# Performance work log

Measured on AMD Instinct MI355X. Metric: run time of the kernel, lower is better.

Reference implementation:

```python
import jax, jax.numpy as jnp
import numpy as np
from jax.scipy.linalg import solve_triangular

B, L, HID, H = 2, 2048, 1024, 4
DK, DV = HID // H, HID // H
CHUNK = 32
CONV_K, FIR_SK, FIR_LK, FIR_WK = 4, 3, 31, 64
GIN = HID + 15 * H   # gate mlp input dim
GH = 2 * HID         # fusion_hidden_mult * hidden
FLOOR_INIT = float(np.log(0.05 / 0.95))


def _l2norm(x):
    return x / jnp.sqrt(jnp.sum(x * x, -1, keepdims=True) + 1e-6)


def _dwconv_causal(x_blc, w_ck):
    # x: [B,L,C], w: [C,K] depthwise causal FIR along L
    K = w_ck.shape[-1]
    x = jnp.moveaxis(x_blc, 1, 2)                      # [B,C,L]
    x = jnp.pad(x, ((0, 0), (0, 0), (K - 1, 0)))
    y = jax.lax.conv_general_dilated(x, w_ck[:, None, :], (1,), 'VALID',
                                     feature_group_count=w_ck.shape[0],
                                     dimension_numbers=('NCH', 'OIH', 'NCH'))
    return jnp.moveaxis(y, 2, 1)


def _delta_rule(q, k, v, beta):
    # q,k: [b,h,L,dk]; v: [b,h,L,dv]; beta: [b,h,L]; L % CHUNK == 0
    b, h, Ll, dk = q.shape
    dv = v.shape[-1]
    n = Ll // CHUNK
    q = _l2norm(q); k = _l2norm(k)
    v = v * beta[..., None]
    kb = k * beta[..., None]
    rs = lambda t: t.reshape(b, h, n, CHUNK, t.shape[-1])
    q, k, v, kb = rs(q), rs(k), rs(v), rs(kb)
    tril_strict = jnp.tril(jnp.ones((CHUNK, CHUNK), bool), -1)
    tril = jnp.tril(jnp.ones((CHUNK, CHUNK), bool), 0)
    # strictly-lower part of (k_beta k^T); inv = (I + A)^{-1} (unit lower-triangular)
    A = jnp.where(tril_strict, kb @ jnp.swapaxes(k, -1, -2), 0.0)
    eye = jnp.eye(CHUNK, dtype=q.dtype)
    inv = solve_triangular(eye + A, jnp.broadcast_to(eye, A.shape), lower=True)
    u = inv @ v    # [b,h,n,c,dv]
    w = inv @ kb   # [b,h,n,c,dk]
    qs, ks, us, ws = (jnp.moveaxis(t, 2, 0) for t in (q, k, u, w))
    S0 = jnp.zeros((b, h, dk, dv), q.dtype)

    def step(S, xs):
        q_i, k_i, u_i, w_i = xs
        attn = jnp.where(tril, q_i @ jnp.swapaxes(k_i, -1, -2), 0.0)
        u_adj = u_i - w_i @ S
        o_i = q_i @ S + attn @ u_adj
        S = S + jnp.swapaxes(k_i, -1, -2) @ u_adj
        return S, o_i

    S, o = jax.lax.scan(step, S0, (qs, ks, us, ws))
    o = jnp.moveaxis(o, 0, 2).reshape(b, h, Ll, dv)
    return o, S


def _stats(x):
    # x: [b,l,h,d] -> concat(mean, rms, max_abs) over d -> [b,l,3h]
    mean = x.mean(-1)
    rms = jnp.sqrt(jnp.clip(jnp.mean(x * x, -1), 1e-8))
    mx = jnp.abs(x).max(-1)
    return jnp.concatenate([mean, rms, mx], -1)


def _forward(hidden_states, q_w, k_w, v_w, b_w, convq_w, convk_w, convv_w,
             fir_s, fir_l, fir_wd, g1_w, g1_b, g2_w, g2_b,
             value_bias, log_temp, floor_logit, onorm_w, o_w):
    b, Ll, _ = hidden_states.shape
    # projections + causal short conv + silu (qk_activation='silu')
    q = jax.nn.silu(_dwconv_causal(hidden_states @ q_w.T, convq_w))
    k = jax.nn.silu(_dwconv_causal(hidden_states @ k_w.T, convk_w))
    v = jax.nn.silu(_dwconv_causal(hidden_states @ v_w.T, convv_w))
    tohd = lambda t: t.reshape(b, Ll, H, -1)
    q, k, v = tohd(q), tohd(k), tohd(v)
    beta = jax.nn.sigmoid(hidden_states @ b_w.T)            # [b,l,h]
    tr = lambda t: jnp.moveaxis(t, 1, 2)
    delta_out, _S = _delta_rule(tr(q), tr(k), tr(v), jnp.moveaxis(beta, 1, 2))
    delta_out = jnp.moveaxis(delta_out, 1, 2)               # [b,l,h,dv]
    # per-head depthwise FIR branches on v
    def fir(x, filt):
        y = _dwconv_causal(x.reshape(b, Ll, H * DV), filt.reshape(H * DV, -1))
        return y.reshape(b, Ll, H, DV)
    short, long_, wide = fir(v, fir_s), fir(v, fir_l), fir(v, fir_wd)
    gate_in = jnp.concatenate([hidden_states, _stats(short), _stats(long_),
                               _stats(wide), _stats(delta_out), _stats(v)], -1)
    hdn = jax.nn.gelu(gate_in @ g1_w.T + g1_b, approximate=False)
    logits = (hdn @ g2_w.T + g2_b).reshape(b, Ll, H, 5)
    logits = logits.at[..., 4].add(value_bias)              # value-branch bias
    logits = logits / jnp.exp(log_temp)[None, None, :, None]
    p = jax.nn.softmax(logits, -1)
    # adaptive floor: context branches each guaranteed >= f per head
    f = jax.nn.sigmoid(floor_logit)[None, None, :, None]    # [1,1,h,1]
    scale = 1.0 - 4.0 * f
    w_ctx = f + scale * p[..., :4]
    w_val = scale * p[..., 4:5]
    o = (w_ctx[..., 0:1] * short + w_ctx[..., 1:2] * long_ +
         w_ctx[..., 2:3] * wide + w_ctx[..., 3:4] * delta_out + w_val * v)
    # per-head RMSNorm + output proj
    o = o * jax.lax.rsqrt(jnp.mean(o * o, -1, keepdims=True) + 1e-5) * onorm_w
    return o.reshape(b, Ll, HID) @ o_w.T


def setup_inputs() -> dict:
    key = jax.random.key(0)
    ks = jax.random.split(key, 16)
    rn = lambda i, shp, s: jax.random.normal(ks[i], shp, jnp.float32) * s
    fir_init = lambda i, K: jnp.zeros((H, DV, K), jnp.float32).at[..., -1].set(1.0) + rn(i, (H, DV, K), 0.02)
    g2_b = jnp.zeros((5 * H,), jnp.float32).at[4::5].set(4.0)
    return {
        'hidden_states': jax.random.normal(ks[0], (B, L, HID), jnp.float32),
        'q_w': rn(1, (HID, HID), 0.02), 'k_w': rn(2, (HID, HID), 0.02),
        'v_w': rn(3, (HID, HID), 0.02), 'b_w': rn(4, (H, HID), 0.02),
        'convq_w': rn(5, (HID, CONV_K), 0.2), 'convk_w': rn(6, (HID, CONV_K), 0.2),
        'convv_w': rn(7, (HID, CONV_K), 0.2),
        'fir_s': fir_init(8, FIR_SK), 'fir_l': fir_init(9, FIR_LK), 'fir_wd': fir_init(10, FIR_WK),
        'g1_w': rn(11, (GH, GIN), 0.02), 'g1_b': jnp.zeros((GH,), jnp.float32),
        'g2_w': rn(12, (5 * H, GH), 0.02), 'g2_b': g2_b,
        'value_bias': jnp.full((H,), 4.0, jnp.float32),
        'log_temp': jnp.zeros((H,), jnp.float32),
        'floor_logit': jnp.full((H,), FLOOR_INIT, jnp.float32),
        'onorm_w': jnp.ones((DV,), jnp.float32),
        'o_w': rn(13, (HID, HID), 0.02),
    }


def reference(hidden_states, q_w, k_w, v_w, b_w, convq_w, convk_w, convv_w,
              fir_s, fir_l, fir_wd, g1_w, g1_b, g2_w, g2_b,
              value_bias, log_temp, floor_logit, onorm_w, o_w):
    return _forward(hidden_states, q_w, k_w, v_w, b_w, convq_w, convk_w, convv_w,
                    fir_s, fir_l, fir_wd, g1_w, g1_b, g2_w, g2_b,
                    value_bias, log_temp, floor_logit, onorm_w, o_w)
```

## Files before the change

### kernel.cpp

```cpp
#include <hip/hip_runtime.h>

#define B_ 2
#define L_ 2048
#define HID_ 1024
#define H_ 4
#define D_ 256
#define NTOK 4096
#define CH 32
#define NCH 64

typedef short s16x8 __attribute__((ext_vector_type(8)));
typedef float f32x4 __attribute__((ext_vector_type(4)));
typedef unsigned short u16;
typedef unsigned int u32;

__device__ __forceinline__ u16 f2b(float f) {
  u32 u = __float_as_uint(f);
  u32 r = (u + 0x7fffu + ((u >> 16) & 1u)) >> 16;
  return (u16)r;
}
__device__ __forceinline__ float b2f(u16 h) { return __uint_as_float((u32)h << 16); }
__device__ __forceinline__ float blo(u32 u) { return __uint_as_float(u << 16); }
__device__ __forceinline__ float bhi(u32 u) { return __uint_as_float(u & 0xffff0000u); }

union U4S8 { uint4 u; s16x8 s; };
__device__ __forceinline__ s16x8 as_s16x8(uint4 u) { U4S8 x; x.u = u; return x.s; }

__global__ __launch_bounds__(256)
void cast5(const float* __restrict__ hs, const float* __restrict__ qw,
           const float* __restrict__ kw, const float* __restrict__ vw,
           const float* __restrict__ ow, u16* __restrict__ out)
{
  const long M4 = (long)NTOK * HID_;
  const long M1 = (long)HID_ * HID_;
  long id = ((long)blockIdx.x * 256 + threadIdx.x) * 4;
  const float* src; long off;
  if (id < M4)               { src = hs; off = id; }
  else if (id < M4 + M1)     { src = qw; off = id - M4; }
  else if (id < M4 + 2 * M1) { src = kw; off = id - M4 - M1; }
  else if (id < M4 + 3 * M1) { src = vw; off = id - M4 - 2 * M1; }
  else                       { src = ow; off = id - M4 - 3 * M1; }
  float4 v = *(const float4*)(src + off);
  ushort4 o;
  o.x = f2b(v.x); o.y = f2b(v.y); o.z = f2b(v.z); o.w = f2b(v.w);
  *(ushort4*)(out + id) = o;
}

template<int ACT>
__global__ __launch_bounds__(256)
void gemm_bf16(const u16* __restrict__ A, const u16* __restrict__ W,
               const float* __restrict__ bias, float* __restrict__ C,
               int M, int N, int K)
{
  __shared__ u16 Als[128][64];
  __shared__ u16 Bls[128][64];
  const int tid = threadIdx.x;
  const int n0 = blockIdx.x * 128;
  const int m0 = blockIdx.y * 128;
  const int l = tid & 63, w = tid >> 6;
  const int wm = w >> 1, wn = w & 1;
  const int r15 = l & 15, g = l >> 4;
  const int srow = tid >> 1, sh = tid & 1;

  f32x4 acc[4][4];
#pragma unroll
  for (int i = 0; i < 4; i++)
#pragma unroll
    for (int j = 0; j < 4; j++) acc[i][j] = (f32x4){0.f, 0.f, 0.f, 0.f};

  const long arowoff = (long)(m0 + srow) * K + sh * 32;
  const long browoff = (long)(n0 + srow) * K + sh * 32;
  uint4 ra[4], rb[4];
#pragma unroll
  for (int j2 = 0; j2 < 4; j2++) {
    ra[j2] = *(const uint4*)(A + arowoff + j2 * 8);
    rb[j2] = *(const uint4*)(W + browoff + j2 * 8);
  }
  const int NS = K >> 6;
  for (int s = 0; s < NS; ++s) {
    __syncthreads();
#pragma unroll
    for (int j2 = 0; j2 < 4; j2++) {
      int slot = (sh * 4 + j2) ^ (srow & 7);
      *(uint4*)&Als[srow][slot * 8] = ra[j2];
      *(uint4*)&Bls[srow][slot * 8] = rb[j2];
    }
    __syncthreads();
    if (s + 1 < NS) {
      long k0 = (long)(s + 1) * 64;
#pragma unroll
      for (int j2 = 0; j2 < 4; j2++) {
        ra[j2] = *(const uint4*)(A + arowoff + k0 + j2 * 8);
        rb[j2] = *(const uint4*)(W + browoff + k0 + j2 * 8);
      }
    }
#pragma unroll
    for (int kk2 = 0; kk2 < 2; kk2++) {
      s16x8 af[4], bf[4];
      int slot = ((kk2 * 4 + g) ^ (r15 & 7)) * 8;
#pragma unroll
      for (int mt = 0; mt < 4; mt++)
        af[mt] = *(const s16x8*)&Als[64 * wm + mt * 16 + r15][slot];
#pragma unroll
      for (int nt = 0; nt < 4; nt++)
        bf[nt] = *(const s16x8*)&Bls[64 * wn + nt * 16 + r15][slot];
#pragma unroll
      for (int mt = 0; mt < 4; mt++)
#pragma unroll
        for (int nt = 0; nt < 4; nt++)
          acc[mt][nt] = __builtin_amdgcn_mfma_f32_16x16x32_bf16(af[mt], bf[nt], acc[mt][nt], 0, 0, 0);
    }
  }

#pragma unroll
  for (int mt = 0; mt < 4; mt++) {
#pragma unroll
    for (int nt = 0; nt < 4; nt++) {
      int m = m0 + 64 * wm + mt * 16 + g * 4;
      int n = n0 + 64 * wn + nt * 16 + r15;
      float bv = (ACT == 1) ? bias[n] : 0.f;
#pragma unroll
      for (int r = 0; r < 4; r++) {
        float v = acc[mt][nt][r];
        if (ACT == 1) {
          v += bv;
          v = 0.5f * v * (1.f + erff(v * 0.70710678118654752f));
        }
        C[(long)(m + r) * N + n] = v;
      }
    }
  }
}

__global__ __launch_bounds__(256)
void conv4_silu3(const float* __restrict__ qkv, const float* __restrict__ wq,
                 const float* __restrict__ wk, const float* __restrict__ wv,
                 float* __restrict__ yq, float* __restrict__ yk, float* __restrict__ yv)
{
  long id = (long)blockIdx.x * 256 + threadIdx.x;
  int col = (int)(id % 3072);
  int tok = (int)(id / 3072);
  int g = col >> 10, c = col & 1023;
  int l = tok & (L_ - 1);
  const float* w4 = (g == 0 ? wq : g == 1 ? wk : wv) + c * 4;
  float s = 0.f;
#pragma unroll
  for (int t = 0; t < 4; t++) {
    int lt = l - 3 + t;
    if (lt >= 0) s += qkv[(long)(tok - 3 + t) * 3072 + col] * w4[t];
  }
  float r = s / (1.f + expf(-s));
  float* y = (g == 0 ? yq : g == 1 ? yk : yv);
  y[(long)tok * HID_ + c] = r;
}

__global__ __launch_bounds__(256)
void beta_proj(const float* __restrict__ hs, const float* __restrict__ bw,
               float* __restrict__ beta)
{
  int id = blockIdx.x * 256 + threadIdx.x;
  int h = id & 3;
  int tok = id >> 2;
  const float4* a = (const float4*)(hs + (long)tok * HID_);
  const float4* w = (const float4*)(bw + (long)h * HID_);
  float s = 0.f;
  for (int k = 0; k < HID_ / 4; k++) {
    float4 av = a[k], wv = w[k];
    s += av.x * wv.x + av.y * wv.y + av.z * wv.z + av.w * wv.w;
  }
  beta[id] = 1.f / (1.f + expf(-s));
}

__global__ __launch_bounds__(256)
void pad_g1w(const float* __restrict__ g1w, u16* __restrict__ out)
{
  int id = blockIdx.x * 256 + threadIdx.x;
  int k = id % 1088;
  int n = id / 1088;
  out[id] = (k < 1084) ? f2b(g1w[(long)n * 1084 + k]) : (u16)0;
}

__global__ __launch_bounds__(256)
void delta_prep(const float* __restrict__ qc, const float* __restrict__ kc,
                const float* __restrict__ vc, const float* __restrict__ beta,
                u16* __restrict__ qn, u16* __restrict__ ktb,
                float* __restrict__ ub, u16* __restrict__ wb,
                u16* __restrict__ attnb, u16* __restrict__ attnlo)
{
  __shared__ float qs[CH][260], ks[CH][260], vs[CH][260];
  __shared__ float Xs[CH][33], As[CH][33];
  __shared__ float red[CH][8];
  __shared__ float bet[CH], nf[CH];

  int bid = blockIdx.x;
  int ci = bid & 63, h = (bid >> 6) & 3, b = bid >> 8;
  int tid = threadIdx.x;
  long tok0 = (long)b * L_ + (long)ci * CH;
  const float* qsrc = qc + tok0 * HID_ + h * D_;
  const float* ksrc = kc + tok0 * HID_ + h * D_;
  const float* vsrc = vc + tok0 * HID_ + h * D_;
  int lr = tid >> 6;
  int dd = (tid & 63) << 2;

#pragma unroll
  for (int it = 0; it < 8; it++) {
    int row = lr + it * 4;
    *(float4*)&qs[row][dd] = *(const float4*)(qsrc + (long)row * HID_ + dd);
    *(float4*)&ks[row][dd] = *(const float4*)(ksrc + (long)row * HID_ + dd);
    *(float4*)&vs[row][dd] = *(const float4*)(vsrc + (long)row * HID_ + dd);
  }
  if (tid < CH) bet[tid] = beta[(tok0 + tid) * H_ + h];
  __syncthreads();

  {
    int c = tid >> 3, p = tid & 7;
    float s = 0.f;
    for (int d = p * 32; d < p * 32 + 32; d++) { float v = qs[c][d]; s += v * v; }
    red[c][p] = s;
  }
  __syncthreads();
  if (tid < CH) {
    float s = 0.f;
    for (int p = 0; p < 8; p++) s += red[tid][p];
    nf[tid] = rsqrtf(s + 1e-6f);
  }
  __syncthreads();
#pragma unroll
  for (int it = 0; it < 8; it++) {
    int row = lr + it * 4;
    float f = nf[row];
    qs[row][dd] *= f; qs[row][dd + 1] *= f; qs[row][dd + 2] *= f; qs[row][dd + 3] *= f;
  }
  {
    int c = tid >> 3, p = tid & 7;
    float s = 0.f;
    for (int d = p * 32; d < p * 32 + 32; d++) { float v = ks[c][d]; s += v * v; }
    red[c][p] = s;
  }
  __syncthreads();
  if (tid < CH) {
    float s = 0.f;
    for (int p = 0; p < 8; p++) s += red[tid][p];
    nf[tid] = rsqrtf(s + 1e-6f);
  }
  __syncthreads();
#pragma unroll
  for (int it = 0; it < 8; it++) {
    int row = lr + it * 4;
    float f = nf[row];
    ks[row][dd] *= f; ks[row][dd + 1] *= f; ks[row][dd + 2] *= f; ks[row][dd + 3] *= f;
  }
  __syncthreads();

  long abase = ((long)(b * H_ + h) * NCH + ci) * (CH * CH);
#pragma unroll 1
  for (int r = 0; r < 4; r++) {
    int oid = tid + 256 * r;
    int i = oid >> 5, jj = oid & 31;
    float skk = 0.f, sqk = 0.f;
    for (int d = 0; d < D_; d += 4) {
      float4 ki = *(const float4*)&ks[i][d];
      float4 kj = *(const float4*)&ks[jj][d];
      float4 qi = *(const float4*)&qs[i][d];
      skk += ki.x * kj.x + ki.y * kj.y + ki.z * kj.z + ki.w * kj.w;
      sqk += qi.x * kj.x + qi.y * kj.y + qi.z * kj.z + qi.w * kj.w;
    }
    As[i][jj] = (jj < i) ? bet[i] * skk : 0.f;
    float sv = (jj <= i) ? sqk : 0.f;
    u16 hi16 = f2b(sv);
    attnb[abase + oid] = hi16;
    attnlo[abase + oid] = f2b(sv - b2f(hi16));
  }
  __syncthreads();

  if (tid < CH) {
    int jj = tid;
    for (int i = 0; i < CH; i++) {
      if (i < jj) { Xs[i][jj] = 0.f; continue; }
      float x = (i == jj) ? 1.f : 0.f;
      for (int m = jj; m < i; m++) x -= As[i][m] * Xs[m][jj];
      Xs[i][jj] = x;
    }
  }
  __syncthreads();

#pragma unroll
  for (int r = 0; r < 4; r++) {
    int oid = tid + 256 * r;
    int i = oid >> 5, m = oid & 31;
    As[i][m] = Xs[i][m] * bet[m];
  }
  __syncthreads();

  long cbase = ((long)(b * H_ + h) * NCH + ci) * (CH * D_);
#pragma unroll 1
  for (int c = 0; c < CH; c++) {
    float su = 0.f, sw = 0.f;
    for (int m = 0; m < CH; m++) {
      float xm = As[c][m];
      su = fmaf(xm, vs[m][tid], su);
      sw = fmaf(xm, ks[m][tid], sw);
    }
    ub[cbase + c * D_ + tid] = su;
    wb[cbase + c * D_ + tid] = f2b(sw);
  }
#pragma unroll 1
  for (int i = 0; i < CH; i++) {
    qn[cbase + i * D_ + tid] = f2b(qs[i][tid]);
  }
  {
    u32 pk[16];
#pragma unroll
    for (int c2 = 0; c2 < 16; c2++) {
      float a = ks[2 * c2][tid], b2 = ks[2 * c2 + 1][tid];
      asm("v_cvt_pk_bf16_f32 %0, %1, %2" : "=v"(pk[c2]) : "v"(a), "v"(b2));
    }
    u16* kq = ktb + ((long)(b * H_ + h) * NCH + ci) * (D_ * CH) + (long)tid * CH;
    *(uint4*)(kq + 0)  = make_uint4(pk[0], pk[1], pk[2], pk[3]);
    *(uint4*)(kq + 8)  = make_uint4(pk[4], pk[5], pk[6], pk[7]);
    *(uint4*)(kq + 16) = make_uint4(pk[8], pk[9], pk[10], pk[11]);
    *(uint4*)(kq + 24) = make_uint4(pk[12], pk[13], pk[14], pk[15]);
  }
}

__device__ __forceinline__ void d2b2(f32x4 Ta, f32x4 Tb, int v, int hi,
                                     s16x8* hiF, s16x8* loF)
{
  const bool tb = (hi >> 1) != 0;
  const int base = v + ((hi & 1) << 5);
  float y[8];
#pragma unroll
  for (int r = 0; r < 4; r++) {
    float a0 = __shfl(Ta[r], base);
    float b0 = __shfl(Tb[r], base);
    float a1 = __shfl(Ta[r], base + 16);
    float b1 = __shfl(Tb[r], base + 16);
    y[r] = tb ? b0 : a0;
    y[4 + r] = tb ? b1 : a1;
  }
  u32 h0, h1, h2, h3;
  asm("v_cvt_pk_bf16_f32 %0, %1, %2" : "=v"(h0) : "v"(y[0]), "v"(y[1]));
  asm("v_cvt_pk_bf16_f32 %0, %1, %2" : "=v"(h1) : "v"(y[2]), "v"(y[3]));
  asm("v_cvt_pk_bf16_f32 %0, %1, %2" : "=v"(h2) : "v"(y[4]), "v"(y[5]));
  asm("v_cvt_pk_bf16_f32 %0, %1, %2" : "=v"(h3) : "v"(y[6]), "v"(y[7]));
  float z0 = y[0] - blo(h0), z1 = y[1] - bhi(h0);
  float z2 = y[2] - blo(h1), z3 = y[3] - bhi(h1);
  float z4 = y[4] - blo(h2), z5 = y[5] - bhi(h2);
  float z6 = y[6] - blo(h3), z7 = y[7] - bhi(h3);
  u32 l0, l1, l2, l3;
  asm("v_cvt_pk_bf16_f32 %0, %1, %2" : "=v"(l0) : "v"(z0), "v"(z1));
  asm("v_cvt_pk_bf16_f32 %0, %1, %2" : "=v"(l1) : "v"(z2), "v"(z3));
  asm("v_cvt_pk_bf16_f32 %0, %1, %2" : "=v"(l2) : "v"(z4), "v"(z5));
  asm("v_cvt_pk_bf16_f32 %0, %1, %2" : "=v"(l3) : "v"(z6), "v"(z7));
  U4S8 xh; xh.u = make_uint4(h0, h1, h2, h3);
  U4S8 xl; xl.u = make_uint4(l0, l1, l2, l3);
  *hiF = xh.s; *loF = xl.s;
}

__global__ __launch_bounds__(64, 1)
void delta_scan(const u16* __restrict__ qn, const u16* __restrict__ ktb,
                const float* __restrict__ ub, const u16* __restrict__ wb,
                const u16* __restrict__ attnb, const u16* __restrict__ attnlo,
                float* __restrict__ dout)
{
  const int bid = blockIdx.x;
  const int sl = bid & 15, h = (bid >> 4) & 3, b = bid >> 6;
  const int l = threadIdx.x;
  const int v = l & 15, hi = l >> 4;
  const int dv0 = sl * 16;
  const long bh = (long)(b * H_ + h);

  f32x4 St[16];
#pragma unroll
  for (int t = 0; t < 16; t++) St[t] = (f32x4){0.f, 0.f, 0.f, 0.f};

  uint4 WfA[2][8], QfA[2][8], WfB[2][8], QfB[2][8];
  uint4 KTf[16], ATh[2], ATl[2];
  float Uld[2][4];

  auto loadWQ = [&](uint4 (&W)[2][8], uint4 (&Q)[2][8], int ci) {
    const long cb = (bh * NCH + ci) * (CH * D_);
#pragma unroll
    for (int mt = 0; mt < 2; mt++)
#pragma unroll
      for (int kt = 0; kt < 8; kt++) {
        const long ro = cb + (long)(mt * 16 + v) * D_ + kt * 32 + hi * 8;
        W[mt][kt] = *(const uint4*)(wb + ro);
        Q[mt][kt] = *(const uint4*)(qn + ro);
      }
  };
  auto loadKT = [&](int ci) {
    const long kb = (bh * NCH + ci) * (D_ * CH);
#pragma unroll
    for (int t = 0; t < 16; t++)
      KTf[t] = *(const uint4*)(ktb + kb + (long)(t * 16 + v) * CH + hi * 8);
  };
  auto loadATU = [&](int ci) {
    const long ab = (bh * NCH + ci) * (CH * CH);
    const long cb = (bh * NCH + ci) * (CH * D_);
#pragma unroll
    for (int mt = 0; mt < 2; mt++) {
      ATh[mt] = *(const uint4*)(attnb + ab + (long)(mt * 16 + v) * CH + hi * 8);
      ATl[mt] = *(const uint4*)(attnlo + ab + (long)(mt * 16 + v) * CH + hi * 8);
    }
#pragma unroll
    for (int mt = 0; mt < 2; mt++)
#pragma unroll
      for (int r = 0; r < 4; r++)
        Uld[mt][r] = ub[cb + (long)(mt * 16 + hi * 4 + r) * D_ + dv0 + v];
  };

  auto step = [&](uint4 (&CW)[2][8], uint4 (&CQ)[2][8],
                  uint4 (&NW)[2][8], uint4 (&NQ)[2][8], int ci) {
    loadWQ(NW, NQ, ci + 1);

    f32x4 awt[2], aqt[2];
#pragma unroll
    for (int mt = 0; mt < 2; mt++) { awt[mt] = (f32x4){0.f,0.f,0.f,0.f}; aqt[mt] = (f32x4){0.f,0.f,0.f,0.f}; }
#pragma unroll
    for (int kt = 0; kt < 8; kt++) {
      s16x8 sh_, sl_;
      d2b2(St[2 * kt], St[2 * kt + 1], v, hi, &sh_, &sl_);
#pragma unroll
      for (int mt = 0; mt < 2; mt++) {
        awt[mt] = __builtin_amdgcn_mfma_f32_16x16x32_bf16(as_s16x8(CW[mt][kt]), sh_, awt[mt], 0, 0, 0);
        awt[mt] = __builtin_amdgcn_mfma_f32_16x16x32_bf16(as_s16x8(CW[mt][kt]), sl_, awt[mt], 0, 0, 0);
        aqt[mt] = __builtin_amdgcn_mfma_f32_16x16x32_bf16(as_s16x8(CQ[mt][kt]), sh_, aqt[mt], 0, 0, 0);
        aqt[mt] = __builtin_amdgcn_mfma_f32_16x16x32_bf16(as_s16x8(CQ[mt][kt]), sl_, aqt[mt], 0, 0, 0);
      }
    }

    f32x4 ua0, ua1;
#pragma unroll
    for (int r = 0; r < 4; r++) { ua0[r] = Uld[0][r] - awt[0][r]; ua1[r] = Uld[1][r] - awt[1][r]; }
    s16x8 UAh, UAl;
    d2b2(ua0, ua1, v, hi, &UAh, &UAl);

    f32x4 ot[2];
#pragma unroll
    for (int mt = 0; mt < 2; mt++) {
      ot[mt] = __builtin_amdgcn_mfma_f32_16x16x32_bf16(as_s16x8(ATh[mt]), UAh, aqt[mt], 0, 0, 0);
      ot[mt] = __builtin_amdgcn_mfma_f32_16x16x32_bf16(as_s16x8(ATh[mt]), UAl, ot[mt], 0, 0, 0);
      ot[mt] = __builtin_amdgcn_mfma_f32_16x16x32_bf16(as_s16x8(ATl[mt]), UAh, ot[mt], 0, 0, 0);
    }
#pragma unroll
    for (int mt = 0; mt < 2; mt++)
#pragma unroll
      for (int r = 0; r < 4; r++)
        dout[((long)b * L_ + ci * CH + mt * 16 + hi * 4 + r) * HID_ + h * D_ + dv0 + v] = ot[mt][r];

    loadATU(ci + 1);

#pragma unroll
    for (int t = 0; t < 16; t++) {
      St[t] = __builtin_amdgcn_mfma_f32_16x16x32_bf16(as_s16x8(KTf[t]), UAh, St[t], 0, 0, 0);
      St[t] = __builtin_amdgcn_mfma_f32_16x16x32_bf16(as_s16x8(KTf[t]), UAl, St[t], 0, 0, 0);
    }
    loadKT(ci + 1);
  };

  loadWQ(WfA, QfA, 0);
  loadKT(0);
  loadATU(0);
#pragma unroll 1
  for (int c2 = 0; c2 < NCH / 2; c2++) {
    step(WfA, QfA, WfB, QfB, 2 * c2);
    step(WfB, QfB, WfA, QfA, 2 * c2 + 1);
  }
}

__global__ __launch_bounds__(256)
void fir3(const float* __restrict__ v, const float* __restrict__ fs_g,
          const float* __restrict__ fl_g, const float* __restrict__ fw_g,
          float* __restrict__ os, float* __restrict__ ol, float* __restrict__ ow)
{
  __shared__ float xs[95][64];
  __shared__ float fs[64][3];
  __shared__ float fl[64][31];
  __shared__ float fw[64][65];
  int bid = blockIdx.x;
  int ct = bid & 15, lt = bid >> 4;
  int c0 = ct * 64, tok0 = lt * 32;
  int bstart = (tok0 / L_) * L_;
  int tid = threadIdx.x;

  for (int idx = tid; idx < 95 * 64; idx += 256) {
    int r = idx >> 6, cc = idx & 63;
    int tok = tok0 - 63 + r;
    xs[r][cc] = (tok >= bstart) ? v[(long)tok * HID_ + c0 + cc] : 0.f;
  }
  for (int idx = tid; idx < 64 * 3; idx += 256) fs[idx / 3][idx % 3] = fs_g[(long)(c0 + idx / 3) * 3 + idx % 3];
  for (int idx = tid; idx < 64 * 31; idx += 256) fl[idx / 31][idx % 31] = fl_g[(long)(c0 + idx / 31) * 31 + idx % 31];
  for (int idx = tid; idx < 64 * 64; idx += 256) fw[idx >> 6][idx & 63] = fw_g[(long)(c0 + (idx >> 6)) * 64 + (idx & 63)];
  __syncthreads();

  int cc = tid & 63, lq = tid >> 6;
  int rb = lq * 8;
  float as8[8] = {0}, al8[8] = {0}, aw8[8] = {0};
#pragma unroll 1
  for (int t = 0; t < 64; t++) {
    float fv = fw[cc][t];
#pragma unroll
    for (int i = 0; i < 8; i++) aw8[i] = fmaf(xs[rb + i + t][cc], fv, aw8[i]);
  }
#pragma unroll 1
  for (int t = 0; t < 31; t++) {
    float fv = fl[cc][t];
#pragma unroll
    for (int i = 0; i < 8; i++) al8[i] = fmaf(xs[rb + 33 + i + t][cc], fv, al8[i]);
  }
#pragma unroll 1
  for (int t = 0; t < 3; t++) {
    float fv = fs[cc][t];
#pragma unroll
    for (int i = 0; i < 8; i++) as8[i] = fmaf(xs[rb + 61 + i + t][cc], fv, as8[i]);
  }
#pragma unroll
  for (int i = 0; i < 8; i++) {
    long o = (long)(tok0 + lq * 8 + i) * HID_ + c0 + cc;
    os[o] = as8[i]; ol[o] = al8[i]; ow[o] = aw8[i];
  }
}

__global__ __launch_bounds__(256)
void build_gate(const float* __restrict__ hs, const float* __restrict__ sb,
                const float* __restrict__ lb, const float* __restrict__ wbb,
                const float* __restrict__ db, const float* __restrict__ vb,
                u16* __restrict__ gate)
{
  int tok = blockIdx.x;
  int tid = threadIdx.x;
  u16* g = gate + (long)tok * 1088;
  const float* hrow = hs + (long)tok * HID_;
#pragma unroll
  for (int i = 0; i < 4; i++) g[tid + 256 * i] = f2b(hrow[tid + 256 * i]);
  if (tid < 4) g[1084 + tid] = 0;
  int h = tid >> 6, ln = tid & 63;
  const float* brs[5] = {sb, lb, wbb, db, vb};
#pragma unroll
  for (int bi = 0; bi < 5; bi++) {
    const float* x = brs[bi] + (long)tok * HID_ + h * D_;
    float s = 0.f, ss = 0.f, mx = 0.f;
#pragma unroll
    for (int i = 0; i < 4; i++) {
      float v = x[ln + 64 * i];
      s += v; ss += v * v; mx = fmaxf(mx, fabsf(v));
    }
#pragma unroll
    for (int off = 32; off >= 1; off >>= 1) {
      s += __shfl_xor(s, off);
      ss += __shfl_xor(ss, off);
      mx = fmaxf(mx, __shfl_xor(mx, off));
    }
    if (ln == 0) {
      g[1024 + bi * 12 + h] = f2b(s * (1.f / 256.f));
      g[1024 + bi * 12 + 4 + h] = f2b(sqrtf(fmaxf(ss * (1.f / 256.f), 1e-8f)));
      g[1024 + bi * 12 + 8 + h] = f2b(mx);
    }
  }
}

__global__ __launch_bounds__(256)
void g2_mix(const float* __restrict__ hdn, const float* __restrict__ g2w,
            const float* __restrict__ g2b, const float* __restrict__ vbias,
            const float* __restrict__ ltemp, const float* __restrict__ flog,
            const float* __restrict__ onw,
            const float* __restrict__ sb, const float* __restrict__ lb,
            const float* __restrict__ wbb, const float* __restrict__ db,
            const float* __restrict__ vb, u16* __restrict__ omix)
{
  __shared__ float hrow[2048];
  __shared__ float lg[20];
  int tok = blockIdx.x;
  int tid = threadIdx.x;
  const float* hp = hdn + (long)tok * 2048;
#pragma unroll
  for (int i = 0; i < 8; i++) hrow[tid + 256 * i] = hp[tid + 256 * i];
  __syncthreads();
  int w = tid >> 6, ln = tid & 63;
#pragma unroll 1
  for (int q = 0; q < 5; q++) {
    int jj = w * 5 + q;
    const float* wr = g2w + (long)jj * 2048;
    float s = 0.f;
    for (int i = 0; i < 32; i++) s += hrow[ln + 64 * i] * wr[ln + 64 * i];
#pragma unroll
    for (int off = 32; off >= 1; off >>= 1) s += __shfl_xor(s, off);
    if (ln == 0) lg[jj] = s + g2b[jj];
  }
  __syncthreads();
  int h = w;
  float l[5];
#pragma unroll
  for (int j = 0; j < 5; j++) l[j] = lg[h * 5 + j];
  l[4] += vbias[h];
  float it = expf(-ltemp[h]);
#pragma unroll
  for (int j = 0; j < 5; j++) l[j] *= it;
  float mx = fmaxf(fmaxf(fmaxf(l[0], l[1]), fmaxf(l[2], l[3])), l[4]);
  float e[5], se = 0.f;
#pragma unroll
  for (int j = 0; j < 5; j++) { e[j] = expf(l[j] - mx); se += e[j]; }
  float inv = 1.f / se;
  float f = 1.f / (1.f + expf(-flog[h]));
  float sc = 1.f - 4.f * f;
  float wt[5];
#pragma unroll
  for (int j = 0; j < 4; j++) wt[j] = f + sc * e[j] * inv;
  wt[4] = sc * e[4] * inv;

  long base = (long)tok * HID_ + h * D_;
  float o[4], ss = 0.f;
#pragma unroll
  for (int i = 0; i < 4; i++) {
    int d = ln + 64 * i;
    o[i] = wt[0] * sb[base + d] + wt[1] * lb[base + d] + wt[2] * wbb[base + d]
         + wt[3] * db[base + d] + wt[4] * vb[base + d];
    ss += o[i] * o[i];
  }
#pragma unroll
  for (int off = 32; off >= 1; off >>= 1) ss += __shfl_xor(ss, off);
  float r = rsqrtf(ss * (1.f / 256.f) + 1e-5f);
#pragma unroll
  for (int i = 0; i < 4; i++) {
    int d = ln + 64 * i;
    omix[base + d] = f2b(o[i] * r * onw[d]);
  }
}

extern "C" void kernel_launch(void* const* d_in, const int* in_sizes, int n_in,
                              void* d_out, int out_size, void* d_ws, size_t ws_size,
                              hipStream_t stream)
{
  const float* hs    = (const float*)d_in[0];
  const float* q_w   = (const float*)d_in[1];
  const float* k_w   = (const float*)d_in[2];
  const float* v_w   = (const float*)d_in[3];
  const float* b_w   = (const float*)d_in[4];
  const float* convq = (const float*)d_in[5];
  const float* convk = (const float*)d_in[6];
  const float* convv = (const float*)d_in[7];
  const float* fir_s = (const float*)d_in[8];
  const float* fir_l = (const float*)d_in[9];
  const float* fir_w = (const float*)d_in[10];
  const float* g1w   = (const float*)d_in[11];
  const float* g1b   = (const float*)d_in[12];
  const float* g2w   = (const float*)d_in[13];
  const float* g2b   = (const float*)d_in[14];
  const float* vbias = (const float*)d_in[15];
  const float* ltemp = (const float*)d_in[16];
  const float* flog  = (const float*)d_in[17];
  const float* onw   = (const float*)d_in[18];
  const float* o_w   = (const float*)d_in[19];

  float* ws = (float*)d_ws;
  const long S1 = (long)NTOK * HID_;
  float* qkv3   = ws + 0 * S1;
  float* qcv    = ws + 3 * S1;
  float* kcv    = ws + 4 * S1;
  float* vcv    = ws + 5 * S1;
  float* ubb    = ws + 6 * S1;
  float* deltab = ws + 7 * S1;
  u16*   qn_bf  = (u16*)(ws + 8 * S1);
  u16*   kt_bf  = (u16*)(ws + 8 * S1 + S1 / 2);
  u16*   wb_bf  = (u16*)(ws + 9 * S1);
  u16*   attn_bf = (u16*)(ws + 9 * S1 + S1 / 2);
  float* betab  = (float*)(attn_bf + (long)B_ * H_ * NCH * CH * CH);
  u16*   attn_lo = (u16*)(betab + 16384);
  u16*   hs_bf  = (u16*)(ws + 10 * S1);
  u16*   qw_bf  = (u16*)(ws + 10 * S1 + S1 / 2);
  u16*   ow_bf  = qw_bf + 3 * (S1 / 4);
  u16*   g1w_bf = ow_bf + S1 / 4;
  float* firs = ws + 0 * S1;
  float* firl = ws + 1 * S1;
  float* firw = ws + 2 * S1;
  u16*   gate_bf = (u16*)qcv;
  u16*   omix_bf = (u16*)kcv;
  float* hdnb    = ws + 8 * S1;
  (void)in_sizes; (void)n_in; (void)out_size; (void)ws_size;

  dim3 blk(256);
  cast5<<<(NTOK * HID_ + 4 * HID_ * HID_) / 1024, blk, 0, stream>>>(hs, q_w, k_w, v_w, o_w, hs_bf);
  pad_g1w<<<2048 * 1088 / 256, blk, 0, stream>>>(g1w, g1w_bf);
  gemm_bf16<0><<<dim3(24, 32), blk, 0, stream>>>(hs_bf, qw_bf, nullptr, qkv3, NTOK, 3072, HID_);
  conv4_silu3<<<(NTOK * 3072) / 256, blk, 0, stream>>>(qkv3, convq, convk, convv, qcv, kcv, vcv);
  beta_proj<<<NTOK * H_ / 256, blk, 0, stream>>>(hs, b_w, betab);
  delta_prep<<<B_ * H_ * NCH, blk, 0, stream>>>(qcv, kcv, vcv, betab, qn_bf, kt_bf, ubb, wb_bf, attn_bf, attn_lo);
  delta_scan<<<B_ * H_ * 16, dim3(64), 0, stream>>>(qn_bf, kt_bf, ubb, wb_bf, attn_bf, attn_lo, deltab);
  fir3<<<(NTOK / 32) * (HID_ / 64), blk, 0, stream>>>(vcv, fir_s, fir_l, fir_w, firs, firl, firw);
  build_gate<<<NTOK, blk, 0, stream>>>(hs, firs, firl, firw, deltab, vcv, gate_bf);
  gemm_bf16<1><<<dim3(16, 32), blk, 0, stream>>>(gate_bf, g1w_bf, g1b, hdnb, NTOK, 2048, 1088);
  g2_mix<<<NTOK, blk, 0, stream>>>(hdnb, g2w, g2b, vbias, ltemp, flog, onw,
                                   firs, firl, firw, deltab, vcv, omix_bf);
  gemm_bf16<0><<<dim3(8, 32), blk, 0, stream>>>(omix_bf, ow_bf, nullptr, (float*)d_out, NTOK, HID_, HID_);
}
```

Before: 886.7 us.

## Move delta_prep chunk matmuls onto bf16 MFMA with split-precision operands

The delta_prep kernel now computes the intra-chunk k·kᵀ and q·kᵀ products with bf16 MFMA instead of scalar fp32 dot products. The u = X·v and w = X·k products also use MFMA, with hi/lo bf16 splits to recover precision, and v and k are transposed into shared memory for this. The q and k norm reductions are merged into one pass using shuffles, and the q bf16 store is folded into the normalization loop. This cuts the scalar FMA work in the prep stage, at the cost of some accuracy in the Gram matrices: k·kᵀ is computed from single bf16 operands, which feed the triangular inverse.

```diff
diff --git a/kernel.cpp b/kernel.cpp
--- a/kernel.cpp
+++ b/kernel.cpp
@@ -25,6 +25,18 @@
 
 union U4S8 { uint4 u; s16x8 s; };
 __device__ __forceinline__ s16x8 as_s16x8(uint4 u) { U4S8 x; x.u = u; return x.s; }
+
+__device__ __forceinline__ u32 pkbf(float a, float b) {
+  u32 r;
+  asm("v_cvt_pk_bf16_f32 %0, %1, %2" : "=v"(r) : "v"(a), "v"(b));
+  return r;
+}
+__device__ __forceinline__ s16x8 cvt8(const float* p) {
+  float4 a = *(const float4*)p;
+  float4 b = *(const float4*)(p + 4);
+  return as_s16x8(make_uint4(pkbf(a.x, a.y), pkbf(a.z, a.w),
+                             pkbf(b.x, b.y), pkbf(b.z, b.w)));
+}
 
 __global__ __launch_bounds__(256)
 void cast5(const float* __restrict__ hs, const float* __restrict__ qw,
@@ -180,6 +192,7 @@
   out[id] = (k < 1084) ? f2b(g1w[(long)n * 1084 + k]) : (u16)0;
 }
 
+#define QSP 264
 __global__ __launch_bounds__(256)
 void delta_prep(const float* __restrict__ qc, const float* __restrict__ kc,
                 const float* __restrict__ vc, const float* __restrict__ beta,
@@ -187,99 +200,157 @@
                 float* __restrict__ ub, u16* __restrict__ wb,
                 u16* __restrict__ attnb, u16* __restrict__ attnlo)
 {
-  __shared__ float qs[CH][260], ks[CH][260], vs[CH][260];
-  __shared__ float Xs[CH][33], As[CH][33];
-  __shared__ float red[CH][8];
-  __shared__ float bet[CH], nf[CH];
-
-  int bid = blockIdx.x;
-  int ci = bid & 63, h = (bid >> 6) & 3, b = bid >> 8;
-  int tid = threadIdx.x;
-  long tok0 = (long)b * L_ + (long)ci * CH;
+  __shared__ float qs_[CH * QSP];
+  __shared__ float ks_[CH * QSP];
+  __shared__ float vs_[CH * QSP];
+  __shared__ u16   kTh[D_ * 40];
+  __shared__ float As[CH][33];
+  __shared__ float Xs[CH][33];
+  __shared__ u16   Xh[CH][40];
+  __shared__ u16   Xl[CH][40];
+  __shared__ float bet[CH], nfq[CH], nfk[CH];
+
+  float* qs = qs_;
+  float* ks = ks_;
+  float* vs = vs_;
+  u16* vTh = (u16*)qs_;
+  u16* vTl = (u16*)ks_;
+
+  const int bid = blockIdx.x;
+  const int ci = bid & 63, h = (bid >> 6) & 3, b = bid >> 8;
+  const int tid = threadIdx.x;
+  const long tok0 = (long)b * L_ + (long)ci * CH;
   const float* qsrc = qc + tok0 * HID_ + h * D_;
   const float* ksrc = kc + tok0 * HID_ + h * D_;
   const float* vsrc = vc + tok0 * HID_ + h * D_;
-  int lr = tid >> 6;
-  int dd = (tid & 63) << 2;
+  const int lr = tid >> 6;
+  const int dd = (tid & 63) << 2;
+  const long cbase = ((long)(b * H_ + h) * NCH + ci) * (CH * D_);
+  const long abase = ((long)(b * H_ + h) * NCH + ci) * (CH * CH);
+  const long kbase = ((long)(b * H_ + h) * NCH + ci) * (D_ * CH);
 
 #pragma unroll
   for (int it = 0; it < 8; it++) {
     int row = lr + it * 4;
-    *(float4*)&qs[row][dd] = *(const float4*)(qsrc + (long)row * HID_ + dd);
-    *(float4*)&ks[row][dd] = *(const float4*)(ksrc + (long)row * HID_ + dd);
-    *(float4*)&vs[row][dd] = *(const float4*)(vsrc + (long)row * HID_ + dd);
+    *(float4*)&qs[row * QSP + dd] = *(const float4*)(qsrc + (long)row * HID_ + dd);
+    *(float4*)&ks[row * QSP + dd] = *(const float4*)(ksrc + (long)row * HID_ + dd);
+    *(float4*)&vs[row * QSP + dd] = *(const float4*)(vsrc + (long)row * HID_ + dd);
   }
   if (tid < CH) bet[tid] = beta[(tok0 + tid) * H_ + h];
   __syncthreads();
 
   {
     int c = tid >> 3, p = tid & 7;
-    float s = 0.f;
-    for (int d = p * 32; d < p * 32 + 32; d++) { float v = qs[c][d]; s += v * v; }
-    red[c][p] = s;
-  }
-  __syncthreads();
-  if (tid < CH) {
-    float s = 0.f;
-    for (int p = 0; p < 8; p++) s += red[tid][p];
-    nf[tid] = rsqrtf(s + 1e-6f);
-  }
-  __syncthreads();
+    const float* qr = qs + c * QSP + p * 32;
+    const float* kr = ks + c * QSP + p * 32;
+    float sq = 0.f, sk = 0.f;
+#pragma unroll
+    for (int i = 0; i < 8; i++) {
+      float4 a = *(const float4*)(qr + i * 4);
+      float4 bq = *(const float4*)(kr + i * 4);
+      sq += a.x * a.x + a.y * a.y + a.z * a.z + a.w * a.w;
+      sk += bq.x * bq.x + bq.y * bq.y + bq.z * bq.z + bq.w * bq.w;
+    }
+#pragma unroll
+    for (int off = 4; off >= 1; off >>= 1) {
+      sq += __shfl_xor(sq, off);
+      sk += __shfl_xor(sk, off);
+    }
+    if (p == 0) { nfq[c] = rsqrtf(sq + 1e-6f); nfk[c] = rsqrtf(sk + 1e-6f); }
+  }
+  __syncthreads();
+
 #pragma unroll
   for (int it = 0; it < 8; it++) {
     int row = lr + it * 4;
-    float f = nf[row];
-    qs[row][dd] *= f; qs[row][dd + 1] *= f; qs[row][dd + 2] *= f; qs[row][dd + 3] *= f;
-  }
+    float fq = nfq[row], fk = nfk[row];
+    float4 qv = *(float4*)&qs[row * QSP + dd];
+    qv.x *= fq; qv.y *= fq; qv.z *= fq; qv.w *= fq;
+    *(float4*)&qs[row * QSP + dd] = qv;
+    ushort4 qo; qo.x = f2b(qv.x); qo.y = f2b(qv.y); qo.z = f2b(qv.z); qo.w = f2b(qv.w);
+    *(ushort4*)(qn + cbase + (long)row * D_ + dd) = qo;
+    float4 kv = *(float4*)&ks[row * QSP + dd];
+    kv.x *= fk; kv.y *= fk; kv.z *= fk; kv.w *= fk;
+    *(float4*)&ks[row * QSP + dd] = kv;
+  }
+  __syncthreads();
+
   {
-    int c = tid >> 3, p = tid & 7;
-    float s = 0.f;
-    for (int d = p * 32; d < p * 32 + 32; d++) { float v = ks[c][d]; s += v * v; }
-    red[c][p] = s;
-  }
-  __syncthreads();
+    const int w = tid >> 6, l = tid & 63;
+    const int v = l & 15, hi = l >> 4;
+    const int ti = w >> 1, tj = w & 1;
+    f32x4 m1 = (f32x4){0.f, 0.f, 0.f, 0.f};
+    f32x4 m2 = (f32x4){0.f, 0.f, 0.f, 0.f};
+#pragma unroll
+    for (int kt = 0; kt < 8; kt++) {
+      const int ko = kt * 32 + hi * 8;
+      s16x8 a1 = cvt8(&ks[(ti * 16 + v) * QSP + ko]);
+      s16x8 a2 = cvt8(&qs[(ti * 16 + v) * QSP + ko]);
+      s16x8 bb = cvt8(&ks[(tj * 16 + v) * QSP + ko]);
+      m1 = __builtin_amdgcn_mfma_f32_16x16x32_bf16(a1, bb, m1, 0, 0, 0);
+      m2 = __builtin_amdgcn_mfma_f32_16x16x32_bf16(a2, bb, m2, 0, 0, 0);
+    }
+#pragma unroll
+    for (int r = 0; r < 4; r++) {
+      int i = ti * 16 + hi * 4 + r, j = tj * 16 + v;
+      As[i][j] = (j < i) ? bet[i] * m1[r] : 0.f;
+      float sv = (j <= i) ? m2[r] : 0.f;
+      u16 hh = f2b(sv);
+      attnb[abase + i * 32 + j] = hh;
+      attnlo[abase + i * 32 + j] = f2b(sv - b2f(hh));
+    }
+  }
+  __syncthreads();
+
+  {
+    u32 pk[16];
+#pragma unroll
+    for (int c2 = 0; c2 < 16; c2++)
+      pk[c2] = pkbf(ks[(2 * c2) * QSP + tid], ks[(2 * c2 + 1) * QSP + tid]);
+    uint4 p0 = make_uint4(pk[0], pk[1], pk[2], pk[3]);
+    uint4 p1 = make_uint4(pk[4], pk[5], pk[6], pk[7]);
+    uint4 p2 = make_uint4(pk[8], pk[9], pk[10], pk[11]);
+    uint4 p3 = make_uint4(pk[12], pk[13], pk[14], pk[15]);
+    *(uint4*)&kTh[tid * 40 + 0]  = p0;
+    *(uint4*)&kTh[tid * 40 + 8]  = p1;
+    *(uint4*)&kTh[tid * 40 + 16] = p2;
+    *(uint4*)&kTh[tid * 40 + 24] = p3;
+    u16* kq = ktb + kbase + (long)tid * CH;
+    *(uint4*)(kq + 0)  = p0;
+    *(uint4*)(kq + 8)  = p1;
+    *(uint4*)(kq + 16) = p2;
+    *(uint4*)(kq + 24) = p3;
+  }
+  __syncthreads();
+
+  {
+    u32 ph[16], pl[16];
+#pragma unroll
+    for (int c2 = 0; c2 < 16; c2++) {
+      float a = vs[(2 * c2) * QSP + tid];
+      float bq = vs[(2 * c2 + 1) * QSP + tid];
+      u32 hp = pkbf(a, bq);
+      ph[c2] = hp;
+      pl[c2] = pkbf(a - blo(hp), bq - bhi(hp));
+    }
+    *(uint4*)&vTh[tid * 40 + 0]  = make_uint4(ph[0], ph[1], ph[2], ph[3]);
+    *(uint4*)&vTh[tid * 40 + 8]  = make_uint4(ph[4], ph[5], ph[6], ph[7]);
+    *(uint4*)&vTh[tid * 40 + 16] = make_uint4(ph[8], ph[9], ph[10], ph[11]);
+    *(uint4*)&vTh[tid * 40 + 24] = make_uint4(ph[12], ph[13], ph[14], ph[15]);
+    *(uint4*)&vTl[tid * 40 + 0]  = make_uint4(pl[0], pl[1], pl[2], pl[3]);
+    *(uint4*)&vTl[tid * 40 + 8]  = make_uint4(pl[4], pl[5], pl[6], pl[7]);
+    *(uint4*)&vTl[tid * 40 + 16] = make_uint4(pl[8], pl[9], pl[10], pl[11]);
+    *(uint4*)&vTl[tid * 40 + 24] = make_uint4(pl[12], pl[13], pl[14], pl[15]);
+  }
+  __syncthreads();
+
   if (tid < CH) {
-    float s = 0.f;
-    for (int p = 0; p < 8; p++) s += red[tid][p];
-    nf[tid] = rsqrtf(s + 1e-6f);
-  }
-  __syncthreads();
-#pragma unroll
-  for (int it = 0; it < 8; it++) {
-    int row = lr + it * 4;
-    float f = nf[row];
-    ks[row][dd] *= f; ks[row][dd + 1] *= f; ks[row][dd + 2] *= f; ks[row][dd + 3] *= f;
-  }
-  __syncthreads();
-
-  long abase = ((long)(b * H_ + h) * NCH + ci) * (CH * CH);
-#pragma unroll 1
-  for (int r = 0; r < 4; r++) {
-    int oid = tid + 256 * r;
-    int i = oid >> 5, jj = oid & 31;
-    float skk = 0.f, sqk = 0.f;
-    for (int d = 0; d < D_; d += 4) {
-      float4 ki = *(const float4*)&ks[i][d];
-      float4 kj = *(const float4*)&ks[jj][d];
-      float4 qi = *(const float4*)&qs[i][d];
-      skk += ki.x * kj.x + ki.y * kj.y + ki.z * kj.z + ki.w * kj.w;
-      sqk += qi.x * kj.x + qi.y * kj.y + qi.z * kj.z + qi.w * kj.w;
-    }
-    As[i][jj] = (jj < i) ? bet[i] * skk : 0.f;
-    float sv = (jj <= i) ? sqk : 0.f;
-    u16 hi16 = f2b(sv);
-    attnb[abase + oid] = hi16;
-    attnlo[abase + oid] = f2b(sv - b2f(hi16));
-  }
-  __syncthreads();
-
-  if (tid < CH) {
-    int jj = tid;
+    int j = tid;
     for (int i = 0; i < CH; i++) {
-      if (i < jj) { Xs[i][jj] = 0.f; continue; }
-      float x = (i == jj) ? 1.f : 0.f;
-      for (int m = jj; m < i; m++) x -= As[i][m] * Xs[m][jj];
-      Xs[i][jj] = x;
+      if (i < j) { Xs[i][j] = 0.f; continue; }
+      float x = (i == j) ? 1.f : 0.f;
+      for (int m = j; m < i; m++) x -= As[i][m] * Xs[m][j];
+      Xs[i][j] = x;
     }
   }
   __syncthreads();
@@ -288,38 +359,40 @@
   for (int r = 0; r < 4; r++) {
     int oid = tid + 256 * r;
     int i = oid >> 5, m = oid & 31;
-    As[i][m] = Xs[i][m] * bet[m];
-  }
-  __syncthreads();
-
-  long cbase = ((long)(b * H_ + h) * NCH + ci) * (CH * D_);
-#pragma unroll 1
-  for (int c = 0; c < CH; c++) {
-    float su = 0.f, sw = 0.f;
-    for (int m = 0; m < CH; m++) {
-      float xm = As[c][m];
-      su = fmaf(xm, vs[m][tid], su);
-      sw = fmaf(xm, ks[m][tid], sw);
-    }
-    ub[cbase + c * D_ + tid] = su;
-    wb[cbase + c * D_ + tid] = f2b(sw);
-  }
-#pragma unroll 1
-  for (int i = 0; i < CH; i++) {
-    qn[cbase + i * D_ + tid] = f2b(qs[i][tid]);
-  }
+    float a2 = Xs[i][m] * bet[m];
+    u16 hh = f2b(a2);
+    Xh[i][m] = hh;
+    Xl[i][m] = f2b(a2 - b2f(hh));
+  }
+  __syncthreads();
+
   {
-    u32 pk[16];
-#pragma unroll
-    for (int c2 = 0; c2 < 16; c2++) {
-      float a = ks[2 * c2][tid], b2 = ks[2 * c2 + 1][tid];
-      asm("v_cvt_pk_bf16_f32 %0, %1, %2" : "=v"(pk[c2]) : "v"(a), "v"(b2));
-    }
-    u16* kq = ktb + ((long)(b * H_ + h) * NCH + ci) * (D_ * CH) + (long)tid * CH;
-    *(uint4*)(kq + 0)  = make_uint4(pk[0], pk[1], pk[2], pk[3]);
-    *(uint4*)(kq + 8)  = make_uint4(pk[4], pk[5], pk[6], pk[7]);
-    *(uint4*)(kq + 16) = make_uint4(pk[8], pk[9], pk[10], pk[11]);
-    *(uint4*)(kq + 24) = make_uint4(pk[12], pk[13], pk[14], pk[15]);
+    const int w = tid >> 6, l = tid & 63;
+    const int v = l & 15, hi = l >> 4;
+    const int ti = w >> 1;
+    const int tjb = (w & 1) * 8;
+    s16x8 xh = *(const s16x8*)&Xh[ti * 16 + v][hi * 8];
+    s16x8 xl = *(const s16x8*)&Xl[ti * 16 + v][hi * 8];
+#pragma unroll
+    for (int tq = 0; tq < 8; tq++) {
+      const int d0 = (tjb + tq) * 16;
+      s16x8 bvh = *(const s16x8*)&vTh[(d0 + v) * 40 + hi * 8];
+      s16x8 bvl = *(const s16x8*)&vTl[(d0 + v) * 40 + hi * 8];
+      s16x8 bkh = *(const s16x8*)&kTh[(d0 + v) * 40 + hi * 8];
+      f32x4 ua = (f32x4){0.f, 0.f, 0.f, 0.f};
+      ua = __builtin_amdgcn_mfma_f32_16x16x32_bf16(xh, bvh, ua, 0, 0, 0);
+      ua = __builtin_amdgcn_mfma_f32_16x16x32_bf16(xh, bvl, ua, 0, 0, 0);
+      ua = __builtin_amdgcn_mfma_f32_16x16x32_bf16(xl, bvh, ua, 0, 0, 0);
+      f32x4 wa = (f32x4){0.f, 0.f, 0.f, 0.f};
+      wa = __builtin_amdgcn_mfma_f32_16x16x32_bf16(xh, bkh, wa, 0, 0, 0);
+      wa = __builtin_amdgcn_mfma_f32_16x16x32_bf16(xl, bkh, wa, 0, 0, 0);
+#pragma unroll
+      for (int r = 0; r < 4; r++) {
+        int c = ti * 16 + hi * 4 + r;
+        ub[cbase + (long)c * D_ + d0 + v] = ua[r];
+        wb[cbase + (long)c * D_ + d0 + v] = f2b(wa[r]);
+      }
+    }
   }
 }
 
@@ -338,20 +411,12 @@
     y[r] = tb ? b0 : a0;
     y[4 + r] = tb ? b1 : a1;
   }
-  u32 h0, h1, h2, h3;
-  asm("v_cvt_pk_bf16_f32 %0, %1, %2" : "=v"(h0) : "v"(y[0]), "v"(y[1]));
-  asm("v_cvt_pk_bf16_f32 %0, %1, %2" : "=v"(h1) : "v"(y[2]), "v"(y[3]));
-  asm("v_cvt_pk_bf16_f32 %0, %1, %2" : "=v"(h2) : "v"(y[4]), "v"(y[5]));
-  asm("v_cvt_pk_bf16_f32 %0, %1, %2" : "=v"(h3) : "v"(y[6]), "v"(y[7]));
-  float z0 = y[0] - blo(h0), z1 = y[1] - bhi(h0);
-  float z2 = y[2] - blo(h1), z3 = y[3] - bhi(h1);
-  float z4 = y[4] - blo(h2), z5 = y[5] - bhi(h2);
-  float z6 = y[6] - blo(h3), z7 = y[7] - bhi(h3);
-  u32 l0, l1, l2, l3;
-  asm("v_cvt_pk_bf16_f32 %0, %1, %2" : "=v"(l0) : "v"(z0), "v"(z1));
-  asm("v_cvt_pk_bf16_f32 %0, %1, %2" : "=v"(l1) : "v"(z2), "v"(z3));
-  asm("v_cvt_pk_bf16_f32 %0, %1, %2" : "=v"(l2) : "v"(z4), "v"(z5));
-  asm("v_cvt_pk_bf16_f32 %0, %1, %2" : "=v"(l3) : "v"(z6), "v"(z7));
+  u32 h0 = pkbf(y[0], y[1]), h1 = pkbf(y[2], y[3]);
+  u32 h2 = pkbf(y[4], y[5]), h3 = pkbf(y[6], y[7]);
+  u32 l0 = pkbf(y[0] - blo(h0), y[1] - bhi(h0));
+  u32 l1 = pkbf(y[2] - blo(h1), y[3] - bhi(h1));
+  u32 l2 = pkbf(y[4] - blo(h2), y[5] - bhi(h2));
+  u32 l3 = pkbf(y[6] - blo(h3), y[7] - bhi(h3));
   U4S8 xh; xh.u = make_uint4(h0, h1, h2, h3);
   U4S8 xl; xl.u = make_uint4(l0, l1, l2, l3);
   *hiF = xh.s; *loF = xl.s;
```

Measured after the change: 840.9 us. 1.05x faster.
